# Kernel tuning notes

Hardware: AMD Instinct MI355X
Metric: run time of the kernel (lower is better)

## Reference

```python
import jax, jax.numpy as jnp
import numpy as np

NODES_PER_GRAPH = 1430  # hard-coded stride in the original forward
GENE0 = 1421            # first gene node index per graph
N_HEADS = 9


def gcn_conv(x, W, b, src, dst, n):
    """PyG-style GCNConv: D^-1/2 (A+I) D^-1/2 X W + b (self-loops added)."""
    h = x @ W  # [N, out]
    ones = jnp.ones(src.shape, jnp.float32)
    deg = jax.ops.segment_sum(ones, dst, num_segments=n) + 1.0  # +1 self-loop
    dinv = jax.lax.rsqrt(deg)
    norm = dinv[src] * dinv[dst]  # [E]
    agg = jax.ops.segment_sum(norm[:, None] * h[src], dst, num_segments=n)
    agg = agg + (dinv * dinv)[:, None] * h  # self-loop contribution
    return agg + b


def setup_inputs() -> dict:
    key = jax.random.key(0)
    ks = jax.random.split(key, 8)
    n_graphs = 512
    n = NODES_PER_GRAPH * n_graphs  # 732160 nodes
    e = n * 8                        # avg degree 8
    x = jax.random.normal(ks[0], (n, 1), jnp.float32)
    edge_index = jax.random.randint(ks[1], (2, e), 0, n, jnp.int32)
    y = jnp.zeros((n_graphs * N_HEADS,), jnp.int32)  # only y.size(0) is used
    W1 = jax.random.normal(ks[2], (1, 16), jnp.float32) * 0.5
    b1 = jnp.zeros((16,), jnp.float32)
    W2 = jax.random.normal(ks[3], (16, 16), jnp.float32) * 0.25
    b2 = jnp.zeros((16,), jnp.float32)
    fw1 = jax.random.normal(ks[4], (N_HEADS, 16, 8), jnp.float32) * 0.25
    fb1 = jnp.zeros((N_HEADS, 8), jnp.float32)
    fw2 = jax.random.normal(ks[5], (N_HEADS, 8, 1), jnp.float32) * 0.35
    fb2 = jnp.zeros((N_HEADS, 1), jnp.float32)
    return {"x": x, "edge_index": edge_index, "y": y, "W1": W1, "b1": b1,
            "W2": W2, "b2": b2, "fw1": fw1, "fb1": fb1, "fw2": fw2, "fb2": fb2}


def reference(x, edge_index, y, W1, b1, W2, b2, fw1, fb1, fw2, fb2):
    n = x.shape[0]
    src, dst = edge_index[0], edge_index[1]
    h = jax.nn.relu(gcn_conv(x, W1, b1, src, dst, n))
    # F.dropout(p=0.4) treated as identity (deterministic eval reference)
    h = jax.nn.relu(gcn_conv(h, W2, b2, src, dst, n))
    n_graphs = y.shape[0] // N_HEADS
    # fused version of the per-gene gather loop: idx[g, k] = 1421+g + k*1430
    idx = (GENE0 + jnp.arange(N_HEADS)[:, None]
           + jnp.arange(n_graphs)[None, :] * NODES_PER_GRAPH)  # [9, G]
    g = h[idx]  # [9, G, 16]
    z = jax.nn.relu(jnp.einsum('gnf,gfh->gnh', g, fw1) + fb1[:, None, :])
    pred = jnp.einsum('gnh,gho->gno', z, fw2) + fb2[:, None, :]  # [9, G, 1]
    return tuple(pred[i] for i in range(N_HEADS))
```

## Files before the change

kernel.cpp:

```cpp
#include <hip/hip_runtime.h>

#define NODES 1430
#define GENE0 1421
#define NHEADS 9
#define BHIST 1024
#define GMAX 64
#define QCAP 1024
#define L1B 1024
#define L1QCAP 3072

__device__ __forceinline__ float frelu(float v) { return v > 0.f ? v : 0.f; }

__global__ __launch_bounds__(BHIST, 4)
void k_hist(const int* __restrict__ esrc, const int* __restrict__ edst,
            unsigned int* __restrict__ copies,
            int* __restrict__ gene_cnt, int* __restrict__ gene_src,
            unsigned int* __restrict__ flagw,
            int e, int K, int R, int n, int hbins, int hwords) {
    extern __shared__ unsigned int lds[];
    int id = blockIdx.x;
    int k, r;
    if ((K & 7) == 0) {
        int xcd = id & 7;
        int slot = id >> 3;
        int cin = slot / R;
        k = xcd * (K >> 3) + cin;
        r = slot - cin * R;
    } else {
        k = id / R;
        r = id - k * R;
    }
    const int tid = threadIdx.x;
    {
        uint4* l4 = (uint4*)lds;
        const int hw4 = hwords >> 2;
        for (int w = tid; w < hw4; w += BHIST) l4[w] = make_uint4(0, 0, 0, 0);
    }
    __syncthreads();

    const unsigned int lo = (unsigned int)r * (unsigned int)hbins;
    const unsigned int hb = (unsigned int)hbins;
    const int e4 = e >> 2;
    const int Q = (e4 + K - 1) / K;
    const int beg = k * Q;
    const int end = min(beg + Q, e4);
    const int4* ed4 = (const int4*)edst;
    const int len = (end > beg) ? (end - beg) : 0;
    const int eighth = len >> 3;

    auto proc = [&](int4 d4) {
#pragma unroll
        for (int c = 0; c < 4; c++) {
            unsigned int d = (unsigned int)((&d4.x)[c]);
            unsigned int rel = d - lo;
            if (rel < hb)
                atomicAdd(&lds[rel >> 3], 1u << ((rel & 7u) * 4u));
        }
    };

    for (int i = tid; i < eighth; i += BHIST) {
        int j0 = beg + i;
        int4 v0 = ed4[j0];
        int4 v1 = ed4[j0 + eighth];
        int4 v2 = ed4[j0 + 2 * eighth];
        int4 v3 = ed4[j0 + 3 * eighth];
        int4 v4 = ed4[j0 + 4 * eighth];
        int4 v5 = ed4[j0 + 5 * eighth];
        int4 v6 = ed4[j0 + 6 * eighth];
        int4 v7 = ed4[j0 + 7 * eighth];
        proc(v0); proc(v1); proc(v2); proc(v3);
        proc(v4); proc(v5); proc(v6); proc(v7);
    }
    for (int i = (eighth << 3) + tid; i < len; i += BHIST) {
        proc(ed4[beg + i]);
    }

    {
        int sbeg = beg + (int)(((long long)len * r) / R);
        int send = beg + (int)(((long long)len * (r + 1)) / R);
        for (int j = sbeg + tid; j < send; j += BHIST) {
            int4 d4 = ed4[j];
#pragma unroll
            for (int c = 0; c < 4; c++) {
                unsigned int d = (unsigned int)((&d4.x)[c]);
                unsigned int graph = d / NODES;
                unsigned int pos = d - graph * NODES;
                if (pos >= GENE0) {
                    int s = esrc[4 * j + c];
                    atomicOr(&flagw[(unsigned)s >> 5], 1u << (s & 31));
                    int g = (int)(graph * NHEADS + (pos - GENE0));
                    int p = atomicAdd(gene_cnt + g, 1);
                    if (p < GMAX) gene_src[(g << 6) + p] = s;
                }
            }
        }
    }

    if (k == 0) {
        for (int j = (e4 << 2) + tid; j < e; j += BHIST) {
            unsigned int d = (unsigned int)edst[j];
            unsigned int rel = d - lo;
            if (rel < hb)
                atomicAdd(&lds[rel >> 3], 1u << ((rel & 7u) * 4u));
            if (r == 0) {
                unsigned int graph = d / NODES;
                unsigned int pos = d - graph * NODES;
                if (pos >= GENE0) {
                    int s = esrc[j];
                    atomicOr(&flagw[(unsigned)s >> 5], 1u << (s & 31));
                    int g = (int)(graph * NHEADS + (pos - GENE0));
                    int p = atomicAdd(gene_cnt + g, 1);
                    if (p < GMAX) gene_src[(g << 6) + p] = s;
                }
            }
        }
    }
    __syncthreads();
    int wlimit = (n > (int)lo) ? ((n - (int)lo + 7) >> 3) : 0;
    if (wlimit > hwords) wlimit = hwords;
    int w4 = (wlimit + 3) >> 2;
    uint4* dst4 = (uint4*)(copies + ((size_t)k * R + r) * hwords);
    const uint4* l4 = (const uint4*)lds;
    for (int w = tid; w < w4; w += BHIST) dst4[w] = l4[w];
}

__global__ void k_reduce(const unsigned int* __restrict__ copies,
                         const float* __restrict__ x,
                         float2* __restrict__ dx, float* __restrict__ t,
                         unsigned int* __restrict__ flagw,
                         int n, int K, int Wtot) {
    int w = blockIdx.x * blockDim.x + threadIdx.x;
    if (w >= Wtot) return;
    int i0 = w << 3;
    if (i0 >= n) return;
    const unsigned int M = 0x0F0F0F0Fu;
    unsigned int ev[8] = {0, 0, 0, 0, 0, 0, 0, 0};
    unsigned int od[8] = {0, 0, 0, 0, 0, 0, 0, 0};
    int k = 0;
    for (; k + 8 <= K; k += 8) {
#pragma unroll
        for (int s = 0; s < 8; s++) {
            unsigned int u = copies[(size_t)(k + s) * Wtot + w];
            ev[s] += u & M; od[s] += (u >> 4) & M;
        }
    }
    for (; k < K; k++) {
        unsigned int u = copies[(size_t)k * Wtot + w];
        ev[0] += u & M; od[0] += (u >> 4) & M;
    }
    unsigned int evn = ((ev[0] + ev[1]) + (ev[2] + ev[3])) + ((ev[4] + ev[5]) + (ev[6] + ev[7]));
    unsigned int odd = ((od[0] + od[1]) + (od[2] + od[3])) + ((od[4] + od[5]) + (od[6] + od[7]));
    float v[8];
#pragma unroll
    for (int b = 0; b < 4; b++) {
        v[2 * b]     = (float)((evn >> (8 * b)) & 0xFFu);
        v[2 * b + 1] = (float)((odd >> (8 * b)) & 0xFFu);
    }
#pragma unroll
    for (int b = 0; b < 8; b++) v[b] = rsqrtf(v[b] + 1.f);
    float4 z4 = {0.f, 0.f, 0.f, 0.f};
    if (i0 + 7 < n) {
        float4 xa = *(const float4*)(x + i0);
        float4 xb = *(const float4*)(x + i0 + 4);
        float4 p0 = {v[0], v[0] * xa.x, v[1], v[1] * xa.y};
        float4 p1 = {v[2], v[2] * xa.z, v[3], v[3] * xa.w};
        float4 p2 = {v[4], v[4] * xb.x, v[5], v[5] * xb.y};
        float4 p3 = {v[6], v[6] * xb.z, v[7], v[7] * xb.w};
        float4* dst = (float4*)(dx + i0);
        dst[0] = p0; dst[1] = p1; dst[2] = p2; dst[3] = p3;
        *(float4*)(t + i0) = z4;
        *(float4*)(t + i0 + 4) = z4;
    } else {
        for (int b = 0; b < 8; b++)
            if (i0 + b < n) {
                float xv = x[i0 + b];
                dx[i0 + b] = make_float2(v[b], v[b] * xv);
                t[i0 + b] = 0.f;
            }
    }
#pragma unroll
    for (int b = 0; b < 8; b++) {
        int i = i0 + b;
        if (i < n) {
            unsigned int graph = (unsigned int)i / NODES;
            unsigned int pos = (unsigned int)i - graph * NODES;
            if (pos >= GENE0) atomicOr(&flagw[(unsigned)i >> 5], 1u << (i & 31));
        }
    }
}

__global__ __launch_bounds__(L1B, 4)
void k_l1_scatter_lds(const int* __restrict__ esrc, const int* __restrict__ edst,
                      const float2* __restrict__ dx,
                      const unsigned int* __restrict__ flagw,
                      float* __restrict__ t, int e, int nw) {
    extern __shared__ unsigned int sh[];
    unsigned int* fl = sh;
    int2* q = (int2*)(sh + ((nw + 3) & ~3));
    __shared__ int qn;
    const int tid = threadIdx.x;
    if (tid == 0) qn = 0;
    {
        const uint4* g4 = (const uint4*)flagw;
        uint4* l4 = (uint4*)fl;
        int nw4 = nw >> 2;
        for (int w = tid; w < nw4; w += L1B) l4[w] = g4[w];
        for (int w = (nw4 << 2) + tid; w < nw; w += L1B) fl[w] = flagw[w];
    }
    __syncthreads();

    const int e4 = e >> 2;
    const int nb = gridDim.x;
    const int Q = (e4 + nb - 1) / nb;
    const int beg = blockIdx.x * Q;
    const int end = min(beg + Q, e4);
    const int len = (end > beg) ? (end - beg) : 0;
    const int4* ed4 = (const int4*)edst;
    const int4* es4 = (const int4*)esrc;

    auto test = [&](int4 dd, int4 ss) {
#pragma unroll
        for (int c = 0; c < 4; c++) {
            int d = (&dd.x)[c];
            if ((fl[(unsigned)d >> 5] >> (d & 31)) & 1u) {
                int p = atomicAdd(&qn, 1);
                if (p < L1QCAP) q[p] = make_int2((&ss.x)[c], d);
                else atomicAdd(t + d, dx[(&ss.x)[c]].y);
            }
        }
    };

    const int quarter = len >> 2;
    for (int i = tid; i < quarter; i += L1B) {
        int j0 = beg + i;
        int4 d0 = ed4[j0],               s0 = es4[j0];
        int4 d1 = ed4[j0 + quarter],     s1 = es4[j0 + quarter];
        int4 d2 = ed4[j0 + 2 * quarter], s2 = es4[j0 + 2 * quarter];
        int4 d3 = ed4[j0 + 3 * quarter], s3 = es4[j0 + 3 * quarter];
        test(d0, s0); test(d1, s1); test(d2, s2); test(d3, s3);
    }
    for (int i = (quarter << 2) + tid; i < len; i += L1B) {
        test(ed4[beg + i], es4[beg + i]);
    }
    if (blockIdx.x == 0) {
        for (int j = (e4 << 2) + tid; j < e; j += L1B) {
            int d = edst[j];
            if ((fl[(unsigned)d >> 5] >> (d & 31)) & 1u)
                atomicAdd(t + d, dx[esrc[j]].y);
        }
    }
    __syncthreads();
    int m = min(qn, L1QCAP);
    for (int i = tid; i < m; i += L1B) {
        int2 sd = q[i];
        atomicAdd(t + sd.y, dx[sd.x].y);
    }
}

__global__ __launch_bounds__(256, 8)
void k_l1_scatter_g(const int* __restrict__ esrc, const int* __restrict__ edst,
                    const float2* __restrict__ dx,
                    const unsigned int* __restrict__ flagw,
                    float* __restrict__ t, int e) {
    __shared__ int2 q[QCAP];
    __shared__ int qn;
    const int tid = threadIdx.x;
    if (tid == 0) qn = 0;
    __syncthreads();

    const int4* ed4 = (const int4*)edst;
    const int4* es4 = (const int4*)esrc;
    const int e4 = e >> 2;
    const int g0 = blockIdx.x * 512;
#pragma unroll
    for (int u = 0; u < 2; u++) {
        int gi = g0 + u * 256 + tid;
        if (gi < e4) {
            int4 dd = ed4[gi];
            int4 ss = es4[gi];
#pragma unroll
            for (int c = 0; c < 4; c++) {
                int d = (&dd.x)[c];
                if ((flagw[(unsigned)d >> 5] >> (d & 31)) & 1u) {
                    int p = atomicAdd(&qn, 1);
                    if (p < QCAP) q[p] = make_int2((&ss.x)[c], d);
                    else atomicAdd(t + d, dx[(&ss.x)[c]].y);
                }
            }
        }
    }
    if (blockIdx.x == 0) {
        for (int j = (e4 << 2) + tid; j < e; j += 256) {
            int d = edst[j];
            if ((flagw[(unsigned)d >> 5] >> (d & 31)) & 1u) {
                int s = esrc[j];
                atomicAdd(t + d, dx[s].y);
            }
        }
    }
    __syncthreads();
    int m = min(qn, QCAP);
    for (int i = tid; i < m; i += 256) {
        int2 sd = q[i];
        atomicAdd(t + sd.y, dx[sd.x].y);
    }
}

__global__ void k_gene_final(const int* __restrict__ gene_cnt, const int* __restrict__ gene_src,
                             const float* __restrict__ t, const float2* __restrict__ dx,
                             const float* __restrict__ W1, const float* __restrict__ b1,
                             const float* __restrict__ W2, const float* __restrict__ b2,
                             const float* __restrict__ fw1, const float* __restrict__ fb1,
                             const float* __restrict__ fw2, const float* __restrict__ fb2,
                             float* __restrict__ out, int NG, int G) {
    int wid = (blockIdx.x * blockDim.x + threadIdx.x) >> 6;
    int lane = threadIdx.x & 63;
    if (wid >= NG) return;
    int g = wid;
    int graph = g / NHEADS;
    int head = g - graph * NHEADS;
    int node = graph * NODES + GENE0 + head;
    const int c = lane & 15;
    const int slot = lane >> 4;

    int cnt = min(gene_cnt[g], GMAX);

    float w1r[16], b1r[16], w2c[16];
#pragma unroll
    for (int kk = 0; kk < 16; kk++) {
        w1r[kk] = W1[kk];
        b1r[kk] = b1[kk];
        w2c[kk] = W2[kk * 16 + c];
    }
    float2 dn2 = dx[node];
    float tn = t[node];

    float acc = 0.f;
    const int base = g << 6;
    for (int i = slot; i < cnt; i += 8) {
        int s0 = gene_src[base + i];
        int i1 = i + 4;
        int s1 = (i1 < cnt) ? gene_src[base + i1] : -1;
        float2 a2 = dx[s0];
        float ta = t[s0];
        float2 b2v = (s1 >= 0) ? dx[s1] : make_float2(0.f, 0.f);
        float tb = (s1 >= 0) ? t[s1] : 0.f;
        {
            float us = a2.x * ta + a2.x * a2.y;
            float m = 0.f;
#pragma unroll
            for (int kk = 0; kk < 16; kk++)
                m += frelu(us * w1r[kk] + b1r[kk]) * w2c[kk];
            acc += a2.x * m;
        }
        if (s1 >= 0) {
            float us = b2v.x * tb + b2v.x * b2v.y;
            float m = 0.f;
#pragma unroll
            for (int kk = 0; kk < 16; kk++)
                m += frelu(us * w1r[kk] + b1r[kk]) * w2c[kk];
            acc += b2v.x * m;
        }
    }
    acc += __shfl_xor(acc, 16, 64);
    acc += __shfl_xor(acc, 32, 64);

    float dn = dn2.x;
    float un = dn * tn + dn * dn2.y;
    float h2 = 0.f;
#pragma unroll
    for (int kk = 0; kk < 16; kk++)
        h2 += frelu(un * w1r[kk] + b1r[kk]) * w2c[kk];
    float h = frelu(dn * acc + dn * dn * h2 + b2[c]);

    float hv[16];
#pragma unroll
    for (int c2 = 0; c2 < 16; c2++) hv[c2] = __shfl(h, c2, 64);

    int kk = lane & 7;
    float z = fb1[head * 8 + kk];
#pragma unroll
    for (int c2 = 0; c2 < 16; c2++) z += hv[c2] * fw1[head * 128 + c2 * 8 + kk];
    float term = frelu(z) * fw2[head * 8 + kk];
    term += __shfl_xor(term, 1, 64);
    term += __shfl_xor(term, 2, 64);
    term += __shfl_xor(term, 4, 64);
    if (lane == 0) out[head * G + graph] = fb2[head] + term;
}

extern "C" void kernel_launch(void* const* d_in, const int* in_sizes, int n_in,
                              void* d_out, int out_size, void* d_ws, size_t ws_size,
                              hipStream_t stream) {
    const float* x   = (const float*)d_in[0];
    const int*   ei  = (const int*)d_in[1];
    const float* W1  = (const float*)d_in[3];
    const float* b1  = (const float*)d_in[4];
    const float* W2  = (const float*)d_in[5];
    const float* b2  = (const float*)d_in[6];
    const float* fw1 = (const float*)d_in[7];
    const float* fb1 = (const float*)d_in[8];
    const float* fw2 = (const float*)d_in[9];
    const float* fb2 = (const float*)d_in[10];

    int n = in_sizes[0];
    int e = in_sizes[1] / 2;
    int G = in_sizes[2] / NHEADS;
    int NG = G * NHEADS;
    const int* esrc = ei;
    const int* edst = ei + e;

    int nw = (n + 31) / 32;
    size_t l1_shmem = (size_t)((nw + 3) & ~3) * 4 + (size_t)L1QCAP * 8;

    static int HB_RT = 0;
    static int L1_LDS_OK = 0;
    if (HB_RT == 0) {
        hipError_t st = hipFuncSetAttribute(
            reinterpret_cast<const void*>(k_hist),
            hipFuncAttributeMaxDynamicSharedMemorySize, 131072);
        HB_RT = (st == hipSuccess) ? 262144 : 131072;
        hipError_t st2 = hipFuncSetAttribute(
            reinterpret_cast<const void*>(k_l1_scatter_lds),
            hipFuncAttributeMaxDynamicSharedMemorySize, (int)l1_shmem);
        L1_LDS_OK = (st2 == hipSuccess && l1_shmem <= 160 * 1024) ? 1 : -1;
    }
    const int HB = HB_RT;
    const int HW = HB >> 3;

    char* ws = (char*)d_ws;
    size_t off = 0;
    auto alloc = [&](size_t bytes) {
        char* p = ws + off;
        off += (bytes + 255) & ~(size_t)255;
        return p;
    };
    int*   gene_cnt      = (int*)alloc((size_t)NG * 4);
    unsigned int* flagw  = (unsigned int*)alloc((size_t)nw * 4);
    size_t zero_bytes    = off;
    int*    gene_src     = (int*)alloc((size_t)NG * GMAX * 4);
    float*  t            = (float*)alloc((size_t)n * 4);
    float2* dx           = (float2*)alloc((size_t)n * 8);
    size_t fixed         = off;

    int R = (n + HB - 1) / HB;
    size_t per_copy = (size_t)R * HW * 4;
    int K = 80;
    if (fixed + (size_t)K * per_copy > ws_size) {
        size_t avail = (ws_size > fixed) ? (ws_size - fixed) : 0;
        int kfit = (int)(avail / per_copy);
        if (kfit >= 8) kfit &= ~7;
        K = kfit < 1 ? 1 : (kfit < K ? kfit : K);
    }
    unsigned int* copies = (unsigned int*)alloc((size_t)K * per_copy);
    (void)n_in; (void)out_size;

    hipMemsetAsync(d_ws, 0, zero_bytes, stream);

    const int B = 256;
    size_t shmem = (size_t)HW * 4;
    k_hist<<<K * R, BHIST, shmem, stream>>>(esrc, edst, copies, gene_cnt, gene_src,
                                            flagw, e, K, R, n, HB, HW);
    int Wtot = R * HW;
    k_reduce<<<(Wtot + B - 1) / B, B, 0, stream>>>(copies, x, dx, t, flagw, n, K, Wtot);
    if (L1_LDS_OK == 1) {
        k_l1_scatter_lds<<<256, L1B, l1_shmem, stream>>>(esrc, edst, dx, flagw, t, e, nw);
    } else {
        int nblk = ((e >> 2) + 511) / 512;
        k_l1_scatter_g<<<nblk, 256, 0, stream>>>(esrc, edst, dx, flagw, t, e);
    }
    int waves_blocks = (NG * 64 + B - 1) / B;
    k_gene_final<<<waves_blocks, B, 0, stream>>>(gene_cnt, gene_src, t, dx,
                                                 W1, b1, W2, b2,
                                                 fw1, fb1, fw2, fb2,
                                                 (float*)d_out, NG, G);
}
```

Baseline: 174.8 us.

## Fold gene-edge detection into histogram pass and lazily load edge sources

The histogram kernel no longer re-reads a slice of destination indices in a separate gene-detection loop. Gene-edge checks now happen inside the per-edge histogram processing, limited to destinations that fall in the block's own bin range. The layer-1 filter kernel stops streaming the whole source array and instead queues edge indices, then fetches the matching sources only for flagged edges before the scatter. This saves a large amount of global bandwidth, at the cost of scattered gathers and one extra barrier.

```diff
diff --git a/kernel.cpp b/kernel.cpp
--- a/kernel.cpp
+++ b/kernel.cpp
@@ -48,13 +48,23 @@
     const int len = (end > beg) ? (end - beg) : 0;
     const int eighth = len >> 3;
 
-    auto proc = [&](int4 d4) {
+    auto proc = [&](int4 d4, int j4) {
 #pragma unroll
         for (int c = 0; c < 4; c++) {
             unsigned int d = (unsigned int)((&d4.x)[c]);
             unsigned int rel = d - lo;
-            if (rel < hb)
+            if (rel < hb) {
                 atomicAdd(&lds[rel >> 3], 1u << ((rel & 7u) * 4u));
+                unsigned int graph = d / NODES;
+                unsigned int pos = d - graph * NODES;
+                if (pos >= GENE0) {
+                    int s = esrc[4 * j4 + c];
+                    atomicOr(&flagw[(unsigned)s >> 5], 1u << (s & 31));
+                    int g = (int)(graph * NHEADS + (pos - GENE0));
+                    int p = atomicAdd(gene_cnt + g, 1);
+                    if (p < GMAX) gene_src[(g << 6) + p] = s;
+                }
+            }
         }
     };
 
@@ -68,41 +78,25 @@
         int4 v5 = ed4[j0 + 5 * eighth];
         int4 v6 = ed4[j0 + 6 * eighth];
         int4 v7 = ed4[j0 + 7 * eighth];
-        proc(v0); proc(v1); proc(v2); proc(v3);
-        proc(v4); proc(v5); proc(v6); proc(v7);
+        proc(v0, j0);
+        proc(v1, j0 + eighth);
+        proc(v2, j0 + 2 * eighth);
+        proc(v3, j0 + 3 * eighth);
+        proc(v4, j0 + 4 * eighth);
+        proc(v5, j0 + 5 * eighth);
+        proc(v6, j0 + 6 * eighth);
+        proc(v7, j0 + 7 * eighth);
     }
     for (int i = (eighth << 3) + tid; i < len; i += BHIST) {
-        proc(ed4[beg + i]);
-    }
-
-    {
-        int sbeg = beg + (int)(((long long)len * r) / R);
-        int send = beg + (int)(((long long)len * (r + 1)) / R);
-        for (int j = sbeg + tid; j < send; j += BHIST) {
-            int4 d4 = ed4[j];
-#pragma unroll
-            for (int c = 0; c < 4; c++) {
-                unsigned int d = (unsigned int)((&d4.x)[c]);
-                unsigned int graph = d / NODES;
-                unsigned int pos = d - graph * NODES;
-                if (pos >= GENE0) {
-                    int s = esrc[4 * j + c];
-                    atomicOr(&flagw[(unsigned)s >> 5], 1u << (s & 31));
-                    int g = (int)(graph * NHEADS + (pos - GENE0));
-                    int p = atomicAdd(gene_cnt + g, 1);
-                    if (p < GMAX) gene_src[(g << 6) + p] = s;
-                }
-            }
-        }
+        proc(ed4[beg + i], beg + i);
     }
 
     if (k == 0) {
         for (int j = (e4 << 2) + tid; j < e; j += BHIST) {
             unsigned int d = (unsigned int)edst[j];
             unsigned int rel = d - lo;
-            if (rel < hb)
+            if (rel < hb) {
                 atomicAdd(&lds[rel >> 3], 1u << ((rel & 7u) * 4u));
-            if (r == 0) {
                 unsigned int graph = d / NODES;
                 unsigned int pos = d - graph * NODES;
                 if (pos >= GENE0) {
@@ -216,16 +210,15 @@
     const int end = min(beg + Q, e4);
     const int len = (end > beg) ? (end - beg) : 0;
     const int4* ed4 = (const int4*)edst;
-    const int4* es4 = (const int4*)esrc;
-
-    auto test = [&](int4 dd, int4 ss) {
+
+    auto test = [&](int4 dd, int j4) {
 #pragma unroll
         for (int c = 0; c < 4; c++) {
             int d = (&dd.x)[c];
             if ((fl[(unsigned)d >> 5] >> (d & 31)) & 1u) {
                 int p = atomicAdd(&qn, 1);
-                if (p < L1QCAP) q[p] = make_int2((&ss.x)[c], d);
-                else atomicAdd(t + d, dx[(&ss.x)[c]].y);
+                if (p < L1QCAP) q[p] = make_int2(4 * j4 + c, d);
+                else atomicAdd(t + d, dx[esrc[4 * j4 + c]].y);
             }
         }
     };
@@ -233,14 +226,17 @@
     const int quarter = len >> 2;
     for (int i = tid; i < quarter; i += L1B) {
         int j0 = beg + i;
-        int4 d0 = ed4[j0],               s0 = es4[j0];
-        int4 d1 = ed4[j0 + quarter],     s1 = es4[j0 + quarter];
-        int4 d2 = ed4[j0 + 2 * quarter], s2 = es4[j0 + 2 * quarter];
-        int4 d3 = ed4[j0 + 3 * quarter], s3 = es4[j0 + 3 * quarter];
-        test(d0, s0); test(d1, s1); test(d2, s2); test(d3, s3);
+        int4 d0 = ed4[j0];
+        int4 d1 = ed4[j0 + quarter];
+        int4 d2 = ed4[j0 + 2 * quarter];
+        int4 d3 = ed4[j0 + 3 * quarter];
+        test(d0, j0);
+        test(d1, j0 + quarter);
+        test(d2, j0 + 2 * quarter);
+        test(d3, j0 + 3 * quarter);
     }
     for (int i = (quarter << 2) + tid; i < len; i += L1B) {
-        test(ed4[beg + i], es4[beg + i]);
+        test(ed4[beg + i], beg + i);
     }
     if (blockIdx.x == 0) {
         for (int j = (e4 << 2) + tid; j < e; j += L1B) {
@@ -251,6 +247,11 @@
     }
     __syncthreads();
     int m = min(qn, L1QCAP);
+    for (int i = tid; i < m; i += L1B) {
+        int2 jd = q[i];
+        q[i].x = esrc[jd.x];
+    }
+    __syncthreads();
     for (int i = tid; i < m; i += L1B) {
         int2 sd = q[i];
         atomicAdd(t + sd.y, dx[sd.x].y);
```

Result: faster. 171.3 us (-2.0%).
